# Optimization experiments

Measured on AMD Instinct MI355X. Metric: run time of the kernel, lower is better.

Reference implementation:

```python
import jax, jax.numpy as jnp
import numpy as np
from jax import lax

# Quantization params from symmetric_linear_quantization_params(num_bits=5, sat=9):
# n = 2**(5-1)-1 = 15, scale = 15/9, zero_point = 0
Q_SCALE = 15.0 / 9.0
Q_ZP = 0.0


def ste_quant_dequant(y, scale=Q_SCALE, zp=Q_ZP):
    # forward: round(scale*y - zp); dequant: (q + zp)/scale. backward: identity (STE).
    q = jnp.round(scale * y - zp)
    dq = (q + zp) / scale
    return y + lax.stop_gradient(dq - y)


def setup_inputs() -> dict:
    key = jax.random.key(0)
    k1, k2, k3 = jax.random.split(key, 3)
    B, Cin, H, Wd = 8, 16, 112, 112
    Cout, KH, KW = 32, 3, 3
    x = jax.random.normal(k1, (B, Cin, H, Wd), dtype=jnp.float32)
    # per-input-channel conv weights: [Cin, Cout, 1, KH, KW]
    W = jax.random.normal(k2, (Cin, Cout, 1, KH, KW), dtype=jnp.float32) * (1.0 / np.sqrt(KH * KW))
    b = jax.random.normal(k3, (Cin, Cout), dtype=jnp.float32) * 0.1
    return {"x": x, "W": W, "b": b}


def reference(x, W, b):
    B, Cin, H, Wd = x.shape
    Cout = W.shape[1]
    # Fuse the in_channels separate 1->Cout convs into one grouped conv:
    # weight [Cin*Cout, 1, KH, KW], feature_group_count=Cin
    w_grouped = W.reshape(Cin * Cout, 1, W.shape[3], W.shape[4])
    y = lax.conv_general_dilated(
        x, w_grouped,
        window_strides=(1, 1),
        padding=((1, 1), (1, 1)),
        dimension_numbers=("NCHW", "OIHW", "NCHW"),
        feature_group_count=Cin,
    )  # [B, Cin*Cout, H, W]
    y = y.reshape(B, Cin, Cout, y.shape[2], y.shape[3])
    y = y + b[None, :, :, None, None]
    # quantize-dequant each per-input-channel partial output, then sum over Cin
    out = jnp.sum(ste_quant_dequant(y), axis=1)  # [B, Cout, H, W]
    return out
```

## Files before the change

### kernel.cpp

```cpp
#include <hip/hip_runtime.h>


typedef float v2f __attribute__((ext_vector_type(2)));

constexpr int B_    = 8;
constexpr int CIN   = 16;
constexpr int COUT  = 32;
constexpr int H_    = 112;
constexpr int W_    = 112;
constexpr int TW    = 16;
constexpr int TH    = 8;
constexpr int LDSW  = 20;
constexpr int HH_   = TH + 2;
constexpr int COG   = 4;

__global__ __launch_bounds__(256, 4)
void conv_quant_sum_kernel(const float* __restrict__ x,
                           const float* __restrict__ w,
                           const float* __restrict__ bias,
                           float* __restrict__ out)
{
#pragma clang fp contract(off)
    const float QS = (float)(15.0 / 9.0);
    const float DQ = 0.6f;

    __shared__ float xs[CIN][HH_][LDSW];

    const int t    = threadIdx.x;
    const int lane = t & 63;
    const int tx   = lane & 7;
    const int ty   = lane >> 3;
    const int wid  = __builtin_amdgcn_readfirstlane(t >> 6);

    const int tile_x = blockIdx.x * TW;
    const int tile_y = blockIdx.y * TH;
    const int b      = blockIdx.z >> 1;
    const int cog    = (blockIdx.z & 1) * 16 + wid * COG;

    const float* xb = x + (size_t)b * CIN * H_ * W_;
    {
        const int sr = t / 20;
        const int sc = t - sr * 20;
        const bool active = (sr < HH_);
        const int gh = tile_y + sr - 1;
        const int gw = tile_x + sc - 1;
        const bool inb = active && ((unsigned)gh < (unsigned)H_) &&
                         ((unsigned)gw < (unsigned)W_);
        const float* sp = inb ? (xb + gh * W_ + gw) : xb;
        float v[CIN];
#pragma unroll
        for (int ci = 0; ci < CIN; ++ci)
            v[ci] = sp[ci * (H_ * W_)];
#pragma unroll
        for (int ci = 0; ci < CIN; ++ci)
            v[ci] = inb ? v[ci] : 0.0f;
        if (active) {
#pragma unroll
            for (int ci = 0; ci < CIN; ++ci)
                xs[ci][sr][sc] = v[ci];
        }
    }
    __syncthreads();

    v2f acc[COG];
#pragma unroll
    for (int co = 0; co < COG; ++co) acc[co] = v2f{0.0f, 0.0f};

    for (int ci = 0; ci < CIN; ++ci) {
        v2f xw[3][3];
#pragma unroll
        for (int r = 0; r < 3; ++r) {
            const float* row = &xs[ci][ty + r][2 * tx];
            v2f p0 = *reinterpret_cast<const v2f*>(row);
            v2f p1 = *reinterpret_cast<const v2f*>(row + 2);
            xw[r][0] = p0;
            xw[r][1] = v2f{p0.y, p1.x};
            xw[r][2] = p1;
        }

        const float* wc = w + (ci * COUT + cog) * 9;
        const float* bc = bias + ci * COUT + cog;
#pragma unroll
        for (int co = 0; co < COG; ++co) {
            v2f s = v2f{0.0f, 0.0f};
#pragma unroll
            for (int k = 0; k < 9; ++k) {
                float wv = wc[co * 9 + k];
                s = __builtin_elementwise_fma(xw[k / 3][k % 3], v2f{wv, wv}, s);
            }
            float bv = bc[co];
            v2f y  = s + v2f{bv, bv};
            v2f tq = y * v2f{QS, QS};
            v2f q;
            q.x = rintf(tq.x);
            q.y = rintf(tq.y);
            acc[co] = __builtin_elementwise_fma(q, v2f{DQ, DQ}, acc[co]);
        }
    }

    float* ob = out + ((size_t)b * COUT + cog) * H_ * W_;
    const int oh = tile_y + ty;
    const int ow = tile_x + 2 * tx;
#pragma unroll
    for (int co = 0; co < COG; ++co)
        *reinterpret_cast<v2f*>(ob + co * H_ * W_ + oh * W_ + ow) = acc[co];
}

extern "C" void kernel_launch(void* const* d_in, const int* in_sizes, int n_in,
                              void* d_out, int out_size, void* d_ws, size_t ws_size,
                              hipStream_t stream)
{
    const float* x    = (const float*)d_in[0];
    const float* w    = (const float*)d_in[1];
    const float* bias = (const float*)d_in[2];
    float* out        = (float*)d_out;

    dim3 grid(W_ / TW, H_ / TH, B_ * 2);
    dim3 block(256);
    conv_quant_sum_kernel<<<grid, block, 0, stream>>>(x, w, bias, out);
}
```

Baseline: 83.95 us.

## Double tile height and compute two output rows per thread

Raises the tile height from 8 to 16 rows. Each thread now computes two vertically adjacent output rows, reusing four LDS rows of input for both, and shares each scalar weight load across two FMA chains. The halo staging becomes a two-pass cooperative load over 18 rows, and the LDS row pitch changes to 22. This cuts LDS reads, weight loads and halo overhead per output, but halves the grid to 784 blocks and raises register pressure, which may reduce occupancy and wave balance across CUs.

```diff
diff --git a/kernel.cpp b/kernel.cpp
--- a/kernel.cpp
+++ b/kernel.cpp
@@ -9,9 +9,9 @@
 constexpr int H_    = 112;
 constexpr int W_    = 112;
 constexpr int TW    = 16;
-constexpr int TH    = 8;
-constexpr int LDSW  = 20;
+constexpr int TH    = 16;
 constexpr int HH_   = TH + 2;
+constexpr int LDSW  = 22;
 constexpr int COG   = 4;
 
 __global__ __launch_bounds__(256, 4)
@@ -29,7 +29,7 @@
     const int t    = threadIdx.x;
     const int lane = t & 63;
     const int tx   = lane & 7;
-    const int ty   = lane >> 3;
+    const int ty2  = lane >> 3;
     const int wid  = __builtin_amdgcn_readfirstlane(t >> 6);
 
     const int tile_x = blockIdx.x * TW;
@@ -39,38 +39,44 @@
 
     const float* xb = x + (size_t)b * CIN * H_ * W_;
     {
-        const int sr = t / 20;
-        const int sc = t - sr * 20;
-        const bool active = (sr < HH_);
-        const int gh = tile_y + sr - 1;
-        const int gw = tile_x + sc - 1;
-        const bool inb = active && ((unsigned)gh < (unsigned)H_) &&
-                         ((unsigned)gw < (unsigned)W_);
-        const float* sp = inb ? (xb + gh * W_ + gw) : xb;
-        float v[CIN];
+        const int sr0 = t / 20,         sc0 = t - sr0 * 20;
+        const int i1  = t + 256;
+        const int sr1 = i1 / 20,        sc1 = i1 - sr1 * 20;
+        const bool a1 = (sr1 < HH_);
+        const int gh0 = tile_y + sr0 - 1, gw0 = tile_x + sc0 - 1;
+        const int gh1 = tile_y + sr1 - 1, gw1 = tile_x + sc1 - 1;
+        const bool in0 = ((unsigned)gh0 < (unsigned)H_) && ((unsigned)gw0 < (unsigned)W_);
+        const bool in1 = a1 && ((unsigned)gh1 < (unsigned)H_) && ((unsigned)gw1 < (unsigned)W_);
+        const float* sp0 = in0 ? (xb + gh0 * W_ + gw0) : xb;
+        const float* sp1 = in1 ? (xb + gh1 * W_ + gw1) : xb;
+        float v0[CIN], v1[CIN];
 #pragma unroll
-        for (int ci = 0; ci < CIN; ++ci)
-            v[ci] = sp[ci * (H_ * W_)];
+        for (int ci = 0; ci < CIN; ++ci) { v0[ci] = sp0[ci * (H_ * W_)];
+                                           v1[ci] = sp1[ci * (H_ * W_)]; }
 #pragma unroll
-        for (int ci = 0; ci < CIN; ++ci)
-            v[ci] = inb ? v[ci] : 0.0f;
-        if (active) {
+        for (int ci = 0; ci < CIN; ++ci) { v0[ci] = in0 ? v0[ci] : 0.0f;
+                                           v1[ci] = in1 ? v1[ci] : 0.0f; }
 #pragma unroll
-            for (int ci = 0; ci < CIN; ++ci)
-                xs[ci][sr][sc] = v[ci];
+        for (int ci = 0; ci < CIN; ++ci) xs[ci][sr0][sc0] = v0[ci];
+        if (a1) {
+#pragma unroll
+            for (int ci = 0; ci < CIN; ++ci) xs[ci][sr1][sc1] = v1[ci];
         }
     }
     __syncthreads();
 
-    v2f acc[COG];
+    v2f acc[COG][2];
 #pragma unroll
-    for (int co = 0; co < COG; ++co) acc[co] = v2f{0.0f, 0.0f};
+    for (int co = 0; co < COG; ++co) {
+        acc[co][0] = v2f{0.0f, 0.0f};
+        acc[co][1] = v2f{0.0f, 0.0f};
+    }
 
     for (int ci = 0; ci < CIN; ++ci) {
-        v2f xw[3][3];
+        v2f xw[4][3];
 #pragma unroll
-        for (int r = 0; r < 3; ++r) {
-            const float* row = &xs[ci][ty + r][2 * tx];
+        for (int r = 0; r < 4; ++r) {
+            const float* row = &xs[ci][2 * ty2 + r][2 * tx];
             v2f p0 = *reinterpret_cast<const v2f*>(row);
             v2f p1 = *reinterpret_cast<const v2f*>(row + 2);
             xw[r][0] = p0;
@@ -82,28 +88,35 @@
         const float* bc = bias + ci * COUT + cog;
 #pragma unroll
         for (int co = 0; co < COG; ++co) {
-            v2f s = v2f{0.0f, 0.0f};
+            v2f s0 = v2f{0.0f, 0.0f};
+            v2f s1 = v2f{0.0f, 0.0f};
 #pragma unroll
             for (int k = 0; k < 9; ++k) {
                 float wv = wc[co * 9 + k];
-                s = __builtin_elementwise_fma(xw[k / 3][k % 3], v2f{wv, wv}, s);
+                v2f wvv = v2f{wv, wv};
+                s0 = __builtin_elementwise_fma(xw[k / 3][k % 3],     wvv, s0);
+                s1 = __builtin_elementwise_fma(xw[k / 3 + 1][k % 3], wvv, s1);
             }
             float bv = bc[co];
-            v2f y  = s + v2f{bv, bv};
-            v2f tq = y * v2f{QS, QS};
-            v2f q;
-            q.x = rintf(tq.x);
-            q.y = rintf(tq.y);
-            acc[co] = __builtin_elementwise_fma(q, v2f{DQ, DQ}, acc[co]);
+            v2f bvv = v2f{bv, bv};
+            v2f y0 = s0 + bvv, y1 = s1 + bvv;
+            v2f t0 = y0 * v2f{QS, QS}, t1 = y1 * v2f{QS, QS};
+            v2f q0, q1;
+            q0.x = rintf(t0.x); q0.y = rintf(t0.y);
+            q1.x = rintf(t1.x); q1.y = rintf(t1.y);
+            acc[co][0] = __builtin_elementwise_fma(q0, v2f{DQ, DQ}, acc[co][0]);
+            acc[co][1] = __builtin_elementwise_fma(q1, v2f{DQ, DQ}, acc[co][1]);
         }
     }
 
     float* ob = out + ((size_t)b * COUT + cog) * H_ * W_;
-    const int oh = tile_y + ty;
+    const int oh = tile_y + 2 * ty2;
     const int ow = tile_x + 2 * tx;
 #pragma unroll
-    for (int co = 0; co < COG; ++co)
-        *reinterpret_cast<v2f*>(ob + co * H_ * W_ + oh * W_ + ow) = acc[co];
+    for (int co = 0; co < COG; ++co) {
+        *reinterpret_cast<v2f*>(ob + co * H_ * W_ + oh * W_ + ow)        = acc[co][0];
+        *reinterpret_cast<v2f*>(ob + co * H_ * W_ + (oh + 1) * W_ + ow)  = acc[co][1];
+    }
 }
 
 extern "C" void kernel_launch(void* const* d_in, const int* in_sizes, int n_in,
```

New measurement: 83.37 us. No clear change (-0.7%).
